# Kernel tuning notes

Hardware: AMD Instinct MI355X
Metric: run time of the kernel (lower is better)

## Reference

```python
import jax, jax.numpy as jnp
import numpy as np

ROPE_BASE = 10000.0

def _rope_cos_sin(T, d, dtype):
    inv_freq = 1.0 / (ROPE_BASE ** (jnp.arange(0, d, 2, dtype=jnp.float32) / d))
    t = jnp.arange(T, dtype=jnp.float32)
    freqs = t[:, None] * inv_freq[None, :]           # [T, d/2]
    emb = jnp.concatenate([freqs, freqs], axis=-1)   # [T, d]
    return jnp.cos(emb).astype(dtype), jnp.sin(emb).astype(dtype)

def _rotate_half(x):
    x1, x2 = jnp.split(x, 2, axis=-1)
    return jnp.concatenate([-x2, x1], axis=-1)

def setup_inputs() -> dict:
    key = jax.random.key(0)
    k1, k2, k3, k4 = jax.random.split(key, 4)
    B, T, C, H = 4, 4096, 1024, 64
    x = jax.random.normal(k1, (B, T, C), dtype=jnp.float32)
    s = 1.0 / np.sqrt(C)
    Wq = jax.random.normal(k2, (H, C), dtype=jnp.float32) * s
    Wk = jax.random.normal(k3, (H, C), dtype=jnp.float32) * s
    Wv = jax.random.normal(k4, (H, C), dtype=jnp.float32) * s
    return {"x": x, "Wq": Wq, "Wk": Wk, "Wv": Wv}

def reference(x, Wq, Wk, Wv):
    B, T, C = x.shape
    H = Wq.shape[0]
    q = jnp.einsum('btc,hc->bth', x, Wq)
    k = jnp.einsum('btc,hc->bth', x, Wk)
    v = jnp.einsum('btc,hc->bth', x, Wv)
    cos, sin = _rope_cos_sin(T, H, x.dtype)
    q = q * cos + _rotate_half(q) * sin
    k = k * cos + _rotate_half(k) * sin
    # NOTE: original scales by dim_model**-0.5 (C), not head_size
    wei = jnp.einsum('bth,bsh->bts', q, k) * (C ** -0.5)
    causal = jnp.tril(jnp.ones((T, T), dtype=bool))
    wei = jnp.where(causal, wei, -jnp.inf)
    wei = jax.nn.softmax(wei, axis=-1)
    # dropout p=0.0 (identity)
    out = jnp.einsum('bts,bsh->bth', wei, v)
    return out
```

## Files before the change

kernel.cpp:

```cpp
#include <hip/hip_runtime.h>
#include <hip/hip_bf16.h>
#include <math.h>

typedef __attribute__((ext_vector_type(8))) __bf16 bf16x8;
typedef __attribute__((ext_vector_type(4))) float f32x4;
typedef __attribute__((ext_vector_type(16))) float f32x16;
typedef __attribute__((ext_vector_type(4))) float float4_t;
typedef __attribute__((ext_vector_type(4))) unsigned int uint4_t;

#define NB 4
#define TSEQ 4096
#define CD 1024
#define HD 64
#define NCH 16
#define CHT 4

static __device__ __forceinline__ unsigned short f2bf(float f) {
    union { float f; unsigned u; } v; v.f = f;
    unsigned r = v.u + 0x7fffu + ((v.u >> 16) & 1u);
    return (unsigned short)(r >> 16);
}
static __device__ __forceinline__ float bf2f(unsigned short u) {
    union { unsigned int i; float f; } v; v.i = ((unsigned int)u) << 16;
    return v.f;
}
static __device__ __forceinline__ unsigned int pk2(float a, float b) {
    union { __bf16 h[2]; unsigned int u; } x;
    x.h[0] = (__bf16)a; x.h[1] = (__bf16)b;
    return x.u;
}

__global__ __launch_bounds__(256) void wcvt_kernel(const float* __restrict__ wq,
                                                   const float* __restrict__ wk,
                                                   const float* __restrict__ wv,
                                                   unsigned short* __restrict__ wb) {
    int i = blockIdx.x * 256 + threadIdx.x;
    int j = i >> 10;
    int col = i & 1023;
    int jb = j >> 4, off = j & 15;
    int sub = ((jb & 1) << 5) | ((jb & 2) << 3);
    int srcrow = (jb < 8) ? (sub + off) : ((jb - 8) * 16 + off);
    const float* src = (jb < 4) ? wq : ((jb < 8) ? wk : wv);
    wb[i] = f2bf(src[srcrow * 1024 + col]);
}

__global__ __launch_bounds__(256) void qkv_kernel(const float* __restrict__ x,
                                                  const unsigned short* __restrict__ wb,
                                                  unsigned short* __restrict__ qo,
                                                  unsigned short* __restrict__ ko,
                                                  unsigned short* __restrict__ vt) {
    __shared__ unsigned short xs[64][72];
    __shared__ unsigned short ws[64][72];
    const int tid = threadIdx.x;
    const int wave = tid >> 6, lane = tid & 63;
    const int lr = lane & 15;
    const int lk = (lane >> 4) << 3;
    const int rowg = (lane >> 4) << 2;
    const int row0 = blockIdx.x * 64;
    const int cbi = blockIdx.y;
    const int cb = cbi * 64;

    f32x4 acc[4];
#pragma unroll
    for (int i = 0; i < 4; ++i) acc[i] = (f32x4){0.f, 0.f, 0.f, 0.f};

    const int sr = tid >> 2;
    const int sc = (tid & 3) << 4;

    for (int k0 = 0; k0 < CD; k0 += 64) {
        __syncthreads();
        {
            const float4_t* s4 =
                reinterpret_cast<const float4_t*>(x + (size_t)(row0 + sr) * CD + k0 + sc);
            alignas(16) unsigned short tmp[16];
#pragma unroll
            for (int j = 0; j < 4; ++j) {
                float4_t f = s4[j];
#pragma unroll
                for (int e = 0; e < 4; ++e) tmp[j * 4 + e] = f2bf(f[e]);
            }
            *reinterpret_cast<uint4_t*>(&xs[sr][sc]) = *reinterpret_cast<const uint4_t*>(&tmp[0]);
            *reinterpret_cast<uint4_t*>(&xs[sr][sc + 8]) = *reinterpret_cast<const uint4_t*>(&tmp[8]);
        }
        {
            const uint4_t* wsrc =
                reinterpret_cast<const uint4_t*>(wb + (size_t)(cb + sr) * CD + k0 + sc);
            *reinterpret_cast<uint4_t*>(&ws[sr][sc]) = wsrc[0];
            *reinterpret_cast<uint4_t*>(&ws[sr][sc + 8]) = wsrc[1];
        }
        __syncthreads();
#pragma unroll
        for (int kk = 0; kk < 2; ++kk) {
            bf16x8 a = *reinterpret_cast<const bf16x8*>(&xs[wave * 16 + lr][kk * 32 + lk]);
#pragma unroll
            for (int c = 0; c < 4; ++c) {
                bf16x8 bfr = *reinterpret_cast<const bf16x8*>(&ws[c * 16 + lr][kk * 32 + lk]);
                acc[c] = __builtin_amdgcn_mfma_f32_16x16x32_bf16(a, bfr, acc[c], 0, 0, 0);
            }
        }
    }

    const int gr0 = row0 + wave * 16 + rowg;
    const int bidx = gr0 >> 12;
    const int tb = gr0 & (TSEQ - 1);
    if (cbi < 2) {
        unsigned short* o = (cbi == 0) ? qo : ko;
        const float sc2 = (cbi == 0) ? 0.045084218764560315f : 1.0f;
        const float l2b = 0.4152410118609215f;
        const float invf0 = exp2f(-(float)lr * l2b);
        const float invf1 = exp2f(-(float)(lr + 16) * l2b);
#pragma unroll
        for (int r = 0; r < 4; ++r) {
            float t = (float)(tb + r);
            float s0, c0, s1, c1;
            sincosf(t * invf0, &s0, &c0);
            sincosf(t * invf1, &s1, &c1);
            size_t ro = (size_t)(gr0 + r) * HD;
            float lo, hi;
            lo = acc[0][r]; hi = acc[1][r];
            o[ro + 0 + lr]  = f2bf((lo * c0 - hi * s0) * sc2);
            o[ro + 32 + lr] = f2bf((hi * c0 + lo * s0) * sc2);
            lo = acc[2][r]; hi = acc[3][r];
            o[ro + 16 + lr] = f2bf((lo * c1 - hi * s1) * sc2);
            o[ro + 48 + lr] = f2bf((hi * c1 + lo * s1) * sc2);
        }
    } else {
#pragma unroll
        for (int r = 0; r < 4; ++r) {
            size_t vbase = (size_t)bidx * HD * TSEQ + (size_t)(tb + r);
            vt[vbase + (size_t)(0 + lr) * TSEQ]  = f2bf(acc[0][r]);
            vt[vbase + (size_t)(16 + lr) * TSEQ] = f2bf(acc[1][r]);
            vt[vbase + (size_t)(32 + lr) * TSEQ] = f2bf(acc[2][r]);
            vt[vbase + (size_t)(48 + lr) * TSEQ] = f2bf(acc[3][r]);
        }
    }
}

__global__ __launch_bounds__(128, 3) void attn_partial(const unsigned short* __restrict__ q,
                                                       const unsigned short* __restrict__ k,
                                                       const unsigned short* __restrict__ vt,
                                                       unsigned short* __restrict__ po,
                                                       float* __restrict__ pm,
                                                       float* __restrict__ pl) {
    const int chunk = blockIdx.x, qt = blockIdx.y, b = blockIdx.z;
    const int kt0 = chunk * CHT;
    if (kt0 > qt) return;
    const int ktend = min(qt, kt0 + CHT - 1);

    __shared__ unsigned short ks[64][72];
    __shared__ unsigned short vs[64][72];
    const int tid = threadIdx.x;
    const int wave = tid >> 6, lane = tid & 63;
    const int l31 = lane & 31;
    const int h = lane >> 5;
    const int h8 = h << 3;
    const int qrow0 = qt * 64 + wave * 32;
    const int qpos = qrow0 + l31;

    const unsigned short* qb_ = q + ((size_t)(b * TSEQ + qpos)) * HD + h8;
    bf16x8 qf[4];
#pragma unroll
    for (int s = 0; s < 4; ++s)
        qf[s] = *reinterpret_cast<const bf16x8*>(qb_ + 16 * s);

    f32x16 oacc[2];
#pragma unroll
    for (int dt = 0; dt < 2; ++dt)
#pragma unroll
        for (int r = 0; r < 16; ++r) oacc[dt][r] = 0.f;
    float mreg = -INFINITY;
    float lsum = 0.f;

    const int srow = tid >> 1;
    const int scol = (tid & 1) << 5;
    const unsigned short* kbase = k + (size_t)b * TSEQ * HD;
    const unsigned short* vbase = vt + (size_t)b * HD * TSEQ;
    uint4_t kr[4], vr[4];
    {
        const int s0l = kt0 * 64;
        const unsigned short* kp = kbase + (size_t)(s0l + srow) * HD + scol;
        const unsigned short* vp = vbase + (size_t)srow * TSEQ + s0l + scol;
#pragma unroll
        for (int j = 0; j < 4; ++j) {
            kr[j] = *reinterpret_cast<const uint4_t*>(kp + 8 * j);
            vr[j] = *reinterpret_cast<const uint4_t*>(vp + 8 * j);
        }
    }

    for (int kt = kt0; kt <= ktend; ++kt) {
        const int s0 = kt * 64;
        __syncthreads();
#pragma unroll
        for (int j = 0; j < 4; ++j) {
            *reinterpret_cast<uint4_t*>(&ks[srow][scol + 8 * j]) = kr[j];
            *reinterpret_cast<uint4_t*>(&vs[srow][scol + 8 * j]) = vr[j];
        }
        __syncthreads();
        if (kt < ktend) {
            const int s0l = s0 + 64;
            const unsigned short* kp = kbase + (size_t)(s0l + srow) * HD + scol;
            const unsigned short* vp = vbase + (size_t)srow * TSEQ + s0l + scol;
#pragma unroll
            for (int j = 0; j < 4; ++j) {
                kr[j] = *reinterpret_cast<const uint4_t*>(kp + 8 * j);
                vr[j] = *reinterpret_cast<const uint4_t*>(vp + 8 * j);
            }
        }

        f32x16 sacc[2];
#pragma unroll
        for (int blk = 0; blk < 2; ++blk)
#pragma unroll
            for (int r = 0; r < 16; ++r) sacc[blk][r] = 0.f;
#pragma unroll
        for (int s = 0; s < 4; ++s) {
            bf16x8 ka = *reinterpret_cast<const bf16x8*>(&ks[l31][16 * s + h8]);
            bf16x8 kb2 = *reinterpret_cast<const bf16x8*>(&ks[32 + l31][16 * s + h8]);
            sacc[0] = __builtin_amdgcn_mfma_f32_32x32x16_bf16(ka, qf[s], sacc[0], 0, 0, 0);
            sacc[1] = __builtin_amdgcn_mfma_f32_32x32x16_bf16(kb2, qf[s], sacc[1], 0, 0, 0);
        }

        if (kt == qt) {
#pragma unroll
            for (int blk = 0; blk < 2; ++blk)
#pragma unroll
                for (int r = 0; r < 16; ++r) {
                    int kvpos = s0 + 32 * blk + (r & 3) + ((r >> 2) << 3) + (h << 2);
                    if (kvpos > qpos) sacc[blk][r] = -INFINITY;
                }
        }

        float mx = -INFINITY;
#pragma unroll
        for (int blk = 0; blk < 2; ++blk)
#pragma unroll
            for (int r = 0; r < 16; ++r) mx = fmaxf(mx, sacc[blk][r]);
        mx = fmaxf(mx, __shfl_xor(mx, 32, 64));
        float mnew = fmaxf(mreg, mx);
        float corr = __builtin_amdgcn_exp2f(mreg - mnew);
        mreg = mnew;
        float psum = 0.f;
        float pvv[2][16];
#pragma unroll
        for (int blk = 0; blk < 2; ++blk)
#pragma unroll
            for (int r = 0; r < 16; ++r) {
                float p = __builtin_amdgcn_exp2f(sacc[blk][r] - mnew);
                pvv[blk][r] = p;
                psum += p;
            }
        psum += __shfl_xor(psum, 32, 64);
        lsum = lsum * corr + psum;
#pragma unroll
        for (int dt = 0; dt < 2; ++dt)
#pragma unroll
            for (int r = 0; r < 16; ++r) oacc[dt][r] *= corr;

        unsigned int cw[2][4][2];
#pragma unroll
        for (int blk = 0; blk < 2; ++blk)
#pragma unroll
            for (int G = 0; G < 4; ++G) {
                cw[blk][G][0] = pk2(pvv[blk][4 * G], pvv[blk][4 * G + 1]);
                cw[blk][G][1] = pk2(pvv[blk][4 * G + 2], pvv[blk][4 * G + 3]);
            }

        const bool hif = (h == 1);
#pragma unroll
        for (int s = 0; s < 4; ++s) {
            const int blk = s >> 1, base = (s & 1) << 1;
            unsigned int a0 = cw[blk][base][0],     a1 = cw[blk][base][1];
            unsigned int b0 = cw[blk][base + 1][0], b1 = cw[blk][base + 1][1];
            unsigned int s0w = hif ? a0 : b0;
            unsigned int s1w = hif ? a1 : b1;
            unsigned int r0 = __shfl_xor(s0w, 32, 64);
            unsigned int r1 = __shfl_xor(s1w, 32, 64);
            uint4_t pw;
            pw[0] = hif ? r0 : a0;
            pw[1] = hif ? r1 : a1;
            pw[2] = hif ? b0 : r0;
            pw[3] = hif ? b1 : r1;
            bf16x8 pfrag = *reinterpret_cast<const bf16x8*>(&pw);
            bf16x8 v0 = *reinterpret_cast<const bf16x8*>(&vs[l31][16 * s + h8]);
            bf16x8 v1 = *reinterpret_cast<const bf16x8*>(&vs[32 + l31][16 * s + h8]);
            oacc[0] = __builtin_amdgcn_mfma_f32_32x32x16_bf16(v0, pfrag, oacc[0], 0, 0, 0);
            oacc[1] = __builtin_amdgcn_mfma_f32_32x32x16_bf16(v1, pfrag, oacc[1], 0, 0, 0);
        }
    }

    const int slot = (((b << 6) + qt) << 4) + chunk;
    unsigned short* pob = po + (size_t)slot * 4096;
#pragma unroll
    for (int dt = 0; dt < 2; ++dt)
#pragma unroll
        for (int r = 0; r < 16; ++r) {
            int d = 32 * dt + (r & 3) + ((r >> 2) << 3) + (h << 2);
            pob[d * 64 + wave * 32 + l31] = f2bf(oacc[dt][r]);
        }
    if (h == 0) {
        pm[slot * 64 + wave * 32 + l31] = mreg;
        pl[slot * 64 + wave * 32 + l31] = lsum;
    }
}

__global__ __launch_bounds__(256) void attn_combine(const unsigned short* __restrict__ po,
                                                    const float* __restrict__ pm,
                                                    const float* __restrict__ pl,
                                                    float* __restrict__ out) {
    __shared__ float sm[64][68];
    const int bq = blockIdx.x;
    const int qt = bq & 63;
    const int nch = (qt >> 2) + 1;
    const int qi = threadIdx.x & 63;
    const int dg = threadIdx.x >> 6;
    const int sbase = bq << 4;

    float M = -INFINITY;
    for (int c = 0; c < nch; ++c) M = fmaxf(M, pm[(sbase + c) * 64 + qi]);
    float L = 0.f;
    float acc[16];
#pragma unroll
    for (int j = 0; j < 16; ++j) acc[j] = 0.f;
    for (int c = 0; c < nch; ++c) {
        int s = sbase + c;
        float w = exp2f(pm[s * 64 + qi] - M);
        L += w * pl[s * 64 + qi];
        const unsigned short* p = po + (size_t)s * 4096 + qi;
#pragma unroll
        for (int j = 0; j < 16; ++j) acc[j] += w * bf2f(p[(dg * 16 + j) * 64]);
    }
    float inv = 1.f / L;
#pragma unroll
    for (int j = 0; j < 16; ++j) sm[qi][dg * 16 + j] = acc[j] * inv;
    __syncthreads();
    const int row = threadIdx.x >> 2;
    const int cg = (threadIdx.x & 3) << 4;
    float4_t* dst = reinterpret_cast<float4_t*>(out + (size_t)bq * 4096 + row * 64 + cg);
#pragma unroll
    for (int v4 = 0; v4 < 4; ++v4) {
        float4_t f;
#pragma unroll
        for (int e = 0; e < 4; ++e) f[e] = sm[row][cg + v4 * 4 + e];
        dst[v4] = f;
    }
}

extern "C" void kernel_launch(void* const* d_in, const int* in_sizes, int n_in,
                              void* d_out, int out_size, void* d_ws, size_t ws_size,
                              hipStream_t stream) {
    const float* x = (const float*)d_in[0];
    const float* wq = (const float*)d_in[1];
    const float* wk = (const float*)d_in[2];
    const float* wv = (const float*)d_in[3];
    float* out = (float*)d_out;

    unsigned short* wb = (unsigned short*)d_ws;
    unsigned short* qb = wb + 3 * HD * CD;
    unsigned short* kb = qb + (size_t)NB * TSEQ * HD;
    unsigned short* vtb = kb + (size_t)NB * TSEQ * HD;
    unsigned short* pob = vtb + (size_t)NB * TSEQ * HD;
    float* pm = (float*)(pob + (size_t)4096 * 4096);
    float* pl = pm + (size_t)4096 * 64;

    wcvt_kernel<<<768, 256, 0, stream>>>(wq, wk, wv, wb);
    qkv_kernel<<<dim3(256, 3), 256, 0, stream>>>(x, wb, qb, kb, vtb);
    attn_partial<<<dim3(NCH, 64, NB), 128, 0, stream>>>(qb, kb, vtb, pob, pm, pl);
    attn_combine<<<NB * 64, 256, 0, stream>>>(pob, pm, pl, out);
}
```

Baseline: 73.31 us.

## Add lazy softmax rescaling, tree reductions, and MFMA priority hints

Skips the running-max update and the rescaling of the output accumulator unless some lane's new max exceeds the stored max by more than a threshold, checked wave-wide. Max and sum reductions become trees instead of serial chains to shorten dependency latency. s_setprio is raised around the MFMA loops so other waves favour issuing matrix instructions. The threshold lets exponentials reach up to about 2^7 before rescaling, which is safe in fp32 but changes rounding slightly.

New measurement: 74.02 us. No clear change (+1.0%).

```diff
diff --git a/kernel.cpp b/kernel.cpp
--- a/kernel.cpp
+++ b/kernel.cpp
@@ -212,6 +212,7 @@
         for (int blk = 0; blk < 2; ++blk)
 #pragma unroll
             for (int r = 0; r < 16; ++r) sacc[blk][r] = 0.f;
+        __builtin_amdgcn_s_setprio(1);
 #pragma unroll
         for (int s = 0; s < 4; ++s) {
             bf16x8 ka = *reinterpret_cast<const bf16x8*>(&ks[l31][16 * s + h8]);
@@ -219,6 +220,7 @@
             sacc[0] = __builtin_amdgcn_mfma_f32_32x32x16_bf16(ka, qf[s], sacc[0], 0, 0, 0);
             sacc[1] = __builtin_amdgcn_mfma_f32_32x32x16_bf16(kb2, qf[s], sacc[1], 0, 0, 0);
         }
+        __builtin_amdgcn_s_setprio(0);
 
         if (kt == qt) {
 #pragma unroll
@@ -230,31 +232,43 @@
                 }
         }
 
-        float mx = -INFINITY;
+        float tm[8];
+#pragma unroll
+        for (int r = 0; r < 8; ++r)
+            tm[r] = fmaxf(fmaxf(sacc[0][r], sacc[0][r + 8]),
+                          fmaxf(sacc[1][r], sacc[1][r + 8]));
+#pragma unroll
+        for (int r = 0; r < 4; ++r) tm[r] = fmaxf(tm[r], tm[r + 4]);
+        float mx = fmaxf(fmaxf(tm[0], tm[1]), fmaxf(tm[2], tm[3]));
+        mx = fmaxf(mx, __shfl_xor(mx, 32, 64));
+
+        const bool newmax = !__all(mx <= mreg + 7.0f);
+        if (newmax) {
+            float mnew = fmaxf(mreg, mx);
+            float corr = __builtin_amdgcn_exp2f(mreg - mnew);
+            mreg = mnew;
+            lsum *= corr;
+#pragma unroll
+            for (int dt = 0; dt < 2; ++dt)
+#pragma unroll
+                for (int r = 0; r < 16; ++r) oacc[dt][r] *= corr;
+        }
+
+        float pvv[2][16];
 #pragma unroll
         for (int blk = 0; blk < 2; ++blk)
 #pragma unroll
-            for (int r = 0; r < 16; ++r) mx = fmaxf(mx, sacc[blk][r]);
-        mx = fmaxf(mx, __shfl_xor(mx, 32, 64));
-        float mnew = fmaxf(mreg, mx);
-        float corr = __builtin_amdgcn_exp2f(mreg - mnew);
-        mreg = mnew;
-        float psum = 0.f;
-        float pvv[2][16];
-#pragma unroll
-        for (int blk = 0; blk < 2; ++blk)
-#pragma unroll
-            for (int r = 0; r < 16; ++r) {
-                float p = __builtin_amdgcn_exp2f(sacc[blk][r] - mnew);
-                pvv[blk][r] = p;
-                psum += p;
-            }
+            for (int r = 0; r < 16; ++r)
+                pvv[blk][r] = __builtin_amdgcn_exp2f(sacc[blk][r] - mreg);
+        float ts[8];
+#pragma unroll
+        for (int r = 0; r < 8; ++r)
+            ts[r] = (pvv[0][r] + pvv[0][r + 8]) + (pvv[1][r] + pvv[1][r + 8]);
+#pragma unroll
+        for (int r = 0; r < 4; ++r) ts[r] += ts[r + 4];
+        float psum = (ts[0] + ts[1]) + (ts[2] + ts[3]);
         psum += __shfl_xor(psum, 32, 64);
-        lsum = lsum * corr + psum;
-#pragma unroll
-        for (int dt = 0; dt < 2; ++dt)
-#pragma unroll
-            for (int r = 0; r < 16; ++r) oacc[dt][r] *= corr;
+        lsum += psum;
 
         unsigned int cw[2][4][2];
 #pragma unroll
@@ -266,6 +280,7 @@
             }
 
         const bool hif = (h == 1);
+        __builtin_amdgcn_s_setprio(1);
 #pragma unroll
         for (int s = 0; s < 4; ++s) {
             const int blk = s >> 1, base = (s & 1) << 1;
@@ -286,6 +301,7 @@
             oacc[0] = __builtin_amdgcn_mfma_f32_32x32x16_bf16(v0, pfrag, oacc[0], 0, 0, 0);
             oacc[1] = __builtin_amdgcn_mfma_f32_32x32x16_bf16(v1, pfrag, oacc[1], 0, 0, 0);
         }
+        __builtin_amdgcn_s_setprio(0);
     }
 
     const int slot = (((b << 6) + qt) << 4) + chunk;
```
